# Kernel optimization log

Measured on AMD Instinct MI355X. Metric: run time of the kernel, lower is better.

The kernel has to match this reference:

```python
import jax, jax.numpy as jnp
import numpy as np
import math

B, N0, DEG = 32, 1584, 4
E = B * N0 * DEG
FIN, HID, EDIM, ROUTE, HEADS = 32, 64, 8, 16, 4
NEG = 0.2  # leaky_relu negative slope (alpha)
K1 = math.ceil(0.8 * N0)   # 1268 nodes/graph after pool1
K2 = math.ceil(0.8 * K1)   # 1015 after pool2
K3 = math.ceil(0.8 * K2)   # 812 after pool3


def _gatv2(x, src, dst, emask, edge_attr, Wl, bl, Wr, br, We, att, bo, num_nodes):
    # PyG GATv2Conv, concat=False (mean over heads), edge_dim, eval mode (no dropout)
    xl = (x @ Wl + bl).reshape(-1, HEADS, HID)            # source transform  [N,H,C]
    xr = (x @ Wr + br).reshape(-1, HEADS, HID)            # target transform  [N,H,C]
    ee = (edge_attr @ We).reshape(-1, HEADS, HID)         # edge transform    [E,H,C]
    m = jax.nn.leaky_relu(xl[src] + xr[dst] + ee, NEG)    # [E,H,C]
    logits = jnp.einsum('ehc,hc->eh', m, att)             # [E,H]
    logits = jnp.where(emask[:, None], logits, -jnp.inf)
    mx = jax.ops.segment_max(logits, dst, num_segments=num_nodes)
    mx = jnp.where(jnp.isfinite(mx), mx, 0.0)             # nodes w/o in-edges
    ex = jnp.where(emask[:, None], jnp.exp(logits - mx[dst]), 0.0)
    den = jax.ops.segment_sum(ex, dst, num_segments=num_nodes)
    alpha = ex / jnp.maximum(den[dst], 1e-16)             # segment softmax over dst
    out = jax.ops.segment_sum(alpha[:, :, None] * xl[src], dst, num_segments=num_nodes)
    return out.mean(axis=1) + bo                          # concat=False -> head mean


def _topk(x, src, dst, emask, w, n_per, k):
    # PyG TopKPooling(ratio=0.8): score = tanh(x.w/||w||); keep top-k per graph,
    # scale kept features by score; keep edges whose endpoints both survive.
    s = jnp.tanh((x @ w) / jnp.linalg.norm(w))            # [B*n_per]
    _, idx = jax.lax.top_k(s.reshape(B, n_per), k)        # [B,k]
    perm = (idx + jnp.arange(B)[:, None] * n_per).reshape(-1)
    x_new = x[perm] * s[perm][:, None]
    new_id = jnp.full((B * n_per,), -1, jnp.int32).at[perm].set(
        jnp.arange(B * k, dtype=jnp.int32))
    nsrc, ndst = new_id[src], new_id[dst]
    m = emask & (nsrc >= 0) & (ndst >= 0)
    return x_new, jnp.where(m, nsrc, 0), jnp.where(m, ndst, 0), m


def _readout(x, k):
    # global mean pool || global max pool (nodes are grouped per graph, k each)
    xb = x.reshape(B, k, HID)
    return jnp.concatenate([xb.mean(1), xb.max(1)], axis=1)


def _forward(x, edge_attr, edge_index,
             g1_Wl, g1_bl, g1_Wr, g1_br, g1_We, g1_att, g1_b,
             g2_Wl, g2_bl, g2_Wr, g2_br, g2_We, g2_att, g2_b,
             g3_Wl, g3_bl, g3_Wr, g3_br, g3_We, g3_att, g3_b,
             p1_w, p2_w, p3_w,
             fc1_W, fc1_b, fc2_W, fc2_b, fc3_W, fc3_b):
    src, dst = edge_index[0], edge_index[1]
    emask = jnp.ones((E,), bool)
    h = jax.nn.relu(_gatv2(x, src, dst, emask, edge_attr,
                           g1_Wl, g1_bl, g1_Wr, g1_br, g1_We, g1_att, g1_b, B * N0))
    h, src, dst, emask = _topk(h, src, dst, emask, p1_w, N0, K1)
    x1 = _readout(h, K1)
    h = jax.nn.relu(_gatv2(h, src, dst, emask, edge_attr,
                           g2_Wl, g2_bl, g2_Wr, g2_br, g2_We, g2_att, g2_b, B * K1))
    h, src, dst, emask = _topk(h, src, dst, emask, p2_w, K1, K2)
    x2 = _readout(h, K2)
    h = jax.nn.relu(_gatv2(h, src, dst, emask, edge_attr,
                           g3_Wl, g3_bl, g3_Wr, g3_br, g3_We, g3_att, g3_b, B * K2))
    h, src, dst, emask = _topk(h, src, dst, emask, p3_w, K2, K3)
    x3 = _readout(h, K3)
    r = x1 + x2 + x3                                      # [B, 2*HID]
    h = jax.nn.relu(r @ fc1_W + fc1_b)
    h = jax.nn.relu(h @ fc2_W + fc2_b)                    # dropout results unused in source
    return jax.nn.softmax(h @ fc3_W + fc3_b, axis=1)      # [B, ROUTE]


def setup_inputs() -> dict:
    key = jax.random.key(0)
    ks = iter(jax.random.split(key, 64))
    def nrm(shape, scale):
        return jax.random.normal(next(ks), shape, jnp.float32) * scale
    x = nrm((B * N0, FIN), 1.0)
    srcl = jax.random.randint(next(ks), (B, N0 * DEG), 0, N0)
    dstl = jax.random.randint(next(ks), (B, N0 * DEG), 0, N0)
    off = (jnp.arange(B) * N0)[:, None]
    edge_index = jnp.stack([(srcl + off).reshape(-1),
                            (dstl + off).reshape(-1)]).astype(jnp.int32)
    edge_attr = nrm((E, EDIM), 1.0)
    batch = jnp.repeat(jnp.arange(B, dtype=jnp.int32), N0)
    inp = {"x": x, "edge_attr": edge_attr, "edge_index": edge_index, "batch": batch}
    for li, fin in ((1, FIN), (2, HID), (3, HID)):
        g = 1.0 / np.sqrt(fin)
        inp[f"g{li}_Wl"] = nrm((fin, HEADS * HID), g)
        inp[f"g{li}_bl"] = nrm((HEADS * HID,), 0.02)
        inp[f"g{li}_Wr"] = nrm((fin, HEADS * HID), g)
        inp[f"g{li}_br"] = nrm((HEADS * HID,), 0.02)
        inp[f"g{li}_We"] = nrm((EDIM, HEADS * HID), 1.0 / np.sqrt(EDIM))
        inp[f"g{li}_att"] = nrm((HEADS, HID), 1.0 / np.sqrt(HID))
        inp[f"g{li}_b"] = nrm((HID,), 0.02)
    for li in (1, 2, 3):
        inp[f"p{li}_w"] = nrm((HID,), 1.0 / np.sqrt(HID))
    for fin, fout, nm in ((2 * HID, HID, "fc1"), (HID, HID, "fc2"), (HID, ROUTE, "fc3")):
        inp[f"{nm}_W"] = nrm((fin, fout), 1.0 / np.sqrt(fin))
        inp[f"{nm}_b"] = nrm((fout,), 0.02)
    return inp


def reference(x, edge_attr, edge_index, batch,
              g1_Wl, g1_bl, g1_Wr, g1_br, g1_We, g1_att, g1_b,
              g2_Wl, g2_bl, g2_Wr, g2_br, g2_We, g2_att, g2_b,
              g3_Wl, g3_bl, g3_Wr, g3_br, g3_We, g3_att, g3_b,
              p1_w, p2_w, p3_w,
              fc1_W, fc1_b, fc2_W, fc2_b, fc3_W, fc3_b):
    # batch is implicit: nodes are laid out grouped per graph with static sizes
    del batch
    return _forward(x, edge_attr, edge_index,
                    g1_Wl, g1_bl, g1_Wr, g1_br, g1_We, g1_att, g1_b,
                    g2_Wl, g2_bl, g2_Wr, g2_br, g2_We, g2_att, g2_b,
                    g3_Wl, g3_bl, g3_Wr, g3_br, g3_We, g3_att, g3_b,
                    p1_w, p2_w, p3_w,
                    fc1_W, fc1_b, fc2_W, fc2_b, fc3_W, fc3_b)
```

## Files before the change

kernel.cpp:

```cpp
#include <hip/hip_runtime.h>

typedef unsigned short u16;
typedef unsigned int u32;
typedef unsigned long long u64;

#define E_TOT 202752
#define NMAX  50688
#define HEADS 4
#define B_    32
#define MAXDEG 32

#define CDIV(a,b) (((a)+(b)-1)/(b))

__device__ __forceinline__ u32 ford(float f) {
  u32 u = __float_as_uint(f);
  return (u & 0x80000000u) ? ~u : (u | 0x80000000u);
}
__device__ __forceinline__ float ford_inv(u32 u) {
  u32 b = (u & 0x80000000u) ? (u ^ 0x80000000u) : ~u;
  return __uint_as_float(b);
}

template <int CTRL>
__device__ __forceinline__ float dpp_mov(float x) {
  return __int_as_float(__builtin_amdgcn_mov_dpp(__float_as_int(x), CTRL, 0xF, 0xF, false));
}
__device__ __forceinline__ float row16_sum(float v) {
  v += dpp_mov<0x121>(v);
  v += dpp_mov<0x122>(v);
  v += dpp_mov<0x124>(v);
  v += dpp_mov<0x128>(v);
  return v;
}

__global__ void k_edge_init_csr(const int* __restrict__ ei, int* __restrict__ src,
                                int* __restrict__ dst, int* __restrict__ em,
                                int* __restrict__ cnt, int* __restrict__ csr) {
  int e = blockIdx.x * blockDim.x + threadIdx.x;
  if (e >= E_TOT) return;
  int s = ei[e], d = ei[E_TOT + e];
  src[e] = s;
  dst[e] = d;
  em[e] = 1;
  int pos = atomicAdd(&cnt[d], 1);
  if (pos < MAXDEG) csr[d * MAXDEG + pos] = e;
}

template <int FIN>
__global__ void k_transform_t(const float* __restrict__ hin,
                              const float* __restrict__ Wl, const float* __restrict__ bl,
                              const float* __restrict__ Wr, const float* __restrict__ br,
                              float* __restrict__ xl, float* __restrict__ xr) {
  __shared__ float xs[FIN][20];
  int n0 = blockIdx.x * 16, j = threadIdx.x;
  for (int t = j; t < 16 * FIN; t += 256) {
    int nd = t >> (FIN == 32 ? 5 : 6), f = t & (FIN - 1);
    xs[f][nd] = hin[(size_t)(n0 + nd) * FIN + f];
  }
  __syncthreads();
  float al[16], ar[16];
  float blv = bl[j], brv = br[j];
#pragma unroll
  for (int t = 0; t < 16; ++t) { al[t] = blv; ar[t] = brv; }
  for (int i = 0; i < FIN; ++i) {
    float wl = Wl[i * 256 + j], wr = Wr[i * 256 + j];
    float4 x0 = *(const float4*)&xs[i][0];
    float4 x1 = *(const float4*)&xs[i][4];
    float4 x2 = *(const float4*)&xs[i][8];
    float4 x3 = *(const float4*)&xs[i][12];
    al[0]  += x0.x * wl; ar[0]  += x0.x * wr;
    al[1]  += x0.y * wl; ar[1]  += x0.y * wr;
    al[2]  += x0.z * wl; ar[2]  += x0.z * wr;
    al[3]  += x0.w * wl; ar[3]  += x0.w * wr;
    al[4]  += x1.x * wl; ar[4]  += x1.x * wr;
    al[5]  += x1.y * wl; ar[5]  += x1.y * wr;
    al[6]  += x1.z * wl; ar[6]  += x1.z * wr;
    al[7]  += x1.w * wl; ar[7]  += x1.w * wr;
    al[8]  += x2.x * wl; ar[8]  += x2.x * wr;
    al[9]  += x2.y * wl; ar[9]  += x2.y * wr;
    al[10] += x2.z * wl; ar[10] += x2.z * wr;
    al[11] += x2.w * wl; ar[11] += x2.w * wr;
    al[12] += x3.x * wl; ar[12] += x3.x * wr;
    al[13] += x3.y * wl; ar[13] += x3.y * wr;
    al[14] += x3.z * wl; ar[14] += x3.z * wr;
    al[15] += x3.w * wl; ar[15] += x3.w * wr;
  }
#pragma unroll
  for (int t = 0; t < 16; ++t) {
    xl[(size_t)(n0 + t) * 256 + j] = al[t];
    xr[(size_t)(n0 + t) * 256 + j] = ar[t];
  }
}

__global__ void k_gat_fused(const int* __restrict__ srcv, const int* __restrict__ cnt,
                            const int* __restrict__ csr, const float* __restrict__ ea,
                            const float* __restrict__ We, const float* __restrict__ att,
                            const float* __restrict__ xl, const float* __restrict__ xr,
                            const float* __restrict__ bias, const float* __restrict__ pwv,
                            float* __restrict__ out, float* __restrict__ sc,
                            int N, int npw) {
  int wid = blockIdx.x * 4 + (threadIdx.x >> 6);
  int lane = threadIdx.x & 63;
  int cg = lane & 15;
  int cb = (lane >> 4) * 64 + cg * 4;
  int n0 = wid * npw, n1 = min(N, n0 + npw);
  if (n0 >= N) return;
  float4 at4 = *(const float4*)(att + cb);
  float4 w0 = *(const float4*)(We + 0 * 256 + cb);
  float4 w1 = *(const float4*)(We + 1 * 256 + cb);
  float4 w2 = *(const float4*)(We + 2 * 256 + cb);
  float4 w3 = *(const float4*)(We + 3 * 256 + cb);
  float4 w4_ = *(const float4*)(We + 4 * 256 + cb);
  float4 w5 = *(const float4*)(We + 5 * 256 + cb);
  float4 w6 = *(const float4*)(We + 6 * 256 + cb);
  float4 w7 = *(const float4*)(We + 7 * 256 + cb);
  float4 bi4 = *(const float4*)(bias + cg * 4);
  float4 pw4 = *(const float4*)(pwv + cg * 4);
  float wn = pw4.x * pw4.x + pw4.y * pw4.y + pw4.z * pw4.z + pw4.w * pw4.w;
  wn += __shfl_xor(wn, 1, 64); wn += __shfl_xor(wn, 2, 64);
  wn += __shfl_xor(wn, 4, 64); wn += __shfl_xor(wn, 8, 64);
  float isq = 1.f / sqrtf(wn);

  for (int n = n0; n < n1; ++n) {
    int deg = min(cnt[n], MAXDEG);
    int e_l = 0, s_l = 0;
    if (lane < deg) { e_l = csr[n * MAXDEG + lane]; s_l = srcv[e_l]; }
    float4 xd4 = *(const float4*)(xr + (size_t)n * 256 + cb);
    float m = -INFINITY, l = 0.f;
    float ox = 0.f, oy = 0.f, oz = 0.f, ow = 0.f;
    for (int i0 = 0; i0 < deg; i0 += 4) {
      int c0 = deg - i0; if (c0 > 4) c0 = 4;
      float4 xs[4], a0[4], a1[4];
#pragma unroll
      for (int j = 0; j < 4; ++j) {
        int idx = (j < c0) ? (i0 + j) : i0;
        int e = __shfl(e_l, idx, 64);
        int s = __shfl(s_l, idx, 64);
        xs[j] = *(const float4*)(xl + (size_t)s * 256 + cb);
        a0[j] = *(const float4*)(ea + (size_t)e * 8);
        a1[j] = *(const float4*)(ea + (size_t)e * 8 + 4);
      }
#pragma unroll
      for (int j = 0; j < 4; ++j) {
        if (j < c0) {
          float e0 = a0[j].x * w0.x + a0[j].y * w1.x + a0[j].z * w2.x + a0[j].w * w3.x
                   + a1[j].x * w4_.x + a1[j].y * w5.x + a1[j].z * w6.x + a1[j].w * w7.x;
          float e1 = a0[j].x * w0.y + a0[j].y * w1.y + a0[j].z * w2.y + a0[j].w * w3.y
                   + a1[j].x * w4_.y + a1[j].y * w5.y + a1[j].z * w6.y + a1[j].w * w7.y;
          float e2 = a0[j].x * w0.z + a0[j].y * w1.z + a0[j].z * w2.z + a0[j].w * w3.z
                   + a1[j].x * w4_.z + a1[j].y * w5.z + a1[j].z * w6.z + a1[j].w * w7.z;
          float e3 = a0[j].x * w0.w + a0[j].y * w1.w + a0[j].z * w2.w + a0[j].w * w3.w
                   + a1[j].x * w4_.w + a1[j].y * w5.w + a1[j].z * w6.w + a1[j].w * w7.w;
          float m0 = xs[j].x + xd4.x + e0; m0 = (m0 >= 0.f) ? m0 : 0.2f * m0;
          float m1 = xs[j].y + xd4.y + e1; m1 = (m1 >= 0.f) ? m1 : 0.2f * m1;
          float m2 = xs[j].z + xd4.z + e2; m2 = (m2 >= 0.f) ? m2 : 0.2f * m2;
          float m3 = xs[j].w + xd4.w + e3; m3 = (m3 >= 0.f) ? m3 : 0.2f * m3;
          float v = at4.x * m0 + at4.y * m1 + at4.z * m2 + at4.w * m3;
          v = row16_sum(v);
          float nm = fmaxf(m, v);
          float scale = __expf(m - nm);
          float p = __expf(v - nm);
          ox = ox * scale + p * xs[j].x;
          oy = oy * scale + p * xs[j].y;
          oz = oz * scale + p * xs[j].z;
          ow = ow * scale + p * xs[j].w;
          l = l * scale + p;
          m = nm;
        }
      }
    }
    float inv = 0.25f / fmaxf(l, 1e-16f);
    float r0 = ox * inv, r1 = oy * inv, r2 = oz * inv, r3 = ow * inv;
    r0 += __shfl_xor(r0, 16, 64); r0 += __shfl_xor(r0, 32, 64);
    r1 += __shfl_xor(r1, 16, 64); r1 += __shfl_xor(r1, 32, 64);
    r2 += __shfl_xor(r2, 16, 64); r2 += __shfl_xor(r2, 32, 64);
    r3 += __shfl_xor(r3, 16, 64); r3 += __shfl_xor(r3, 32, 64);
    float rr0 = fmaxf(r0 + bi4.x, 0.f), rr1 = fmaxf(r1 + bi4.y, 0.f);
    float rr2 = fmaxf(r2 + bi4.z, 0.f), rr3 = fmaxf(r3 + bi4.w, 0.f);
    if (lane < 16) *(float4*)(out + (size_t)n * 64 + cg * 4) = float4{rr0, rr1, rr2, rr3};
    float dot = rr0 * pw4.x + rr1 * pw4.y + rr2 * pw4.z + rr3 * pw4.w;
    dot += __shfl_xor(dot, 1, 64);
    dot += __shfl_xor(dot, 2, 64);
    dot += __shfl_xor(dot, 4, 64);
    dot += __shfl_xor(dot, 8, 64);
    if (lane == 0) sc[n] = tanhf(dot * isq);
  }
}

__global__ __launch_bounds__(1024) void k_topk(const float* __restrict__ s, int n_per,
                                               int k, int npad,
                                               int* __restrict__ perm, int* __restrict__ new_id) {
  __shared__ u64 kv[2048];
  int b = blockIdx.x, tid = threadIdx.x;
  int base = b * n_per;
  for (int i = tid; i < n_per; i += 1024) new_id[base + i] = -1;
  for (int i = tid; i < npad; i += 1024) {
    u32 sk = (i < n_per) ? ford(s[base + i]) : 0u;
    kv[i] = ((u64)sk << 32) | (u32)(0xFFFFFFFFu - (u32)i);
  }
  __syncthreads();
  for (int kk = 2; kk <= npad; kk <<= 1) {
    for (int j = kk >> 1; j > 0; j >>= 1) {
      for (int i = tid; i < npad; i += 1024) {
        int ixj = i ^ j;
        if (ixj > i) {
          u64 a = kv[i], c = kv[ixj];
          bool after = a < c;
          bool doswap = ((i & kk) == 0) ? after : !after;
          if (doswap) { kv[i] = c; kv[ixj] = a; }
        }
      }
      __syncthreads();
    }
  }
  for (int r = tid; r < k; r += 1024) {
    int old = (int)(0xFFFFFFFFu - (u32)(kv[r] & 0xFFFFFFFFu));
    perm[b * k + r] = base + old;
    new_id[base + old] = b * k + r;
  }
}

__global__ void k_gather_ro(const float* __restrict__ hin, const float* __restrict__ s,
                            const int* __restrict__ perm, float* __restrict__ hout,
                            int k, float* __restrict__ rsum, u32* __restrict__ rmaxI) {
  __shared__ float ps[256], pm[256];
  int b = blockIdx.x, t = threadIdx.x;
  int i = blockIdx.y * 4 + (t >> 6);
  int c = t & 63;
  bool valid = i < k;
  float v = 0.f;
  if (valid) {
    int g = perm[b * k + i];
    v = hin[(size_t)g * 64 + c] * s[g];
    hout[((size_t)b * k + i) * 64 + c] = v;
  }
  ps[t] = valid ? v : 0.f;
  pm[t] = valid ? v : -INFINITY;
  __syncthreads();
  if (t < 64) {
    float s4 = ps[t] + ps[t + 64] + ps[t + 128] + ps[t + 192];
    float m4 = fmaxf(fmaxf(pm[t], pm[t + 64]), fmaxf(pm[t + 128], pm[t + 192]));
    atomicAdd(&rsum[b * 64 + t], s4);
    atomicMax(&rmaxI[b * 64 + t], ford(m4));
  }
}

__global__ void k_remap_csr(int* __restrict__ src, int* __restrict__ dst,
                            int* __restrict__ em, const int* __restrict__ new_id,
                            int* __restrict__ cnt, int* __restrict__ csr) {
  int e = blockIdx.x * blockDim.x + threadIdx.x;
  if (e >= E_TOT) return;
  int ns = new_id[src[e]], nd = new_id[dst[e]];
  int m = em[e] && ns >= 0 && nd >= 0;
  src[e] = m ? ns : 0;
  dst[e] = m ? nd : 0;
  em[e] = m;
  if (m) {
    int pos = atomicAdd(&cnt[nd], 1);
    if (pos < MAXDEG) csr[nd * MAXDEG + pos] = e;
  }
}

__global__ void k_mlp(const char* __restrict__ rblk,
                      const float* __restrict__ W1, const float* __restrict__ b1,
                      const float* __restrict__ W2, const float* __restrict__ b2,
                      const float* __restrict__ W3, const float* __restrict__ b3,
                      float* __restrict__ out) {
  __shared__ float v0[128], v1[64], v2[64], lgts[16];
  int b = blockIdx.x, t = threadIdx.x;
  const float* rs0 = (const float*)rblk;
  const u32*   rm0 = (const u32*)(rblk + 32 * 64 * 4);
  const float* rs1 = (const float*)(rblk + 32 * 128 * 4);
  const u32*   rm1 = (const u32*)(rblk + 32 * 128 * 4 + 32 * 64 * 4);
  const float* rs2 = (const float*)(rblk + 2 * 32 * 128 * 4);
  const u32*   rm2 = (const u32*)(rblk + 2 * 32 * 128 * 4 + 32 * 64 * 4);
  v0[t] = rs0[b * 64 + t] / 1268.f + rs1[b * 64 + t] / 1015.f + rs2[b * 64 + t] / 812.f;
  v0[64 + t] = ford_inv(rm0[b * 64 + t]) + ford_inv(rm1[b * 64 + t]) + ford_inv(rm2[b * 64 + t]);
  __syncthreads();
  float a = b1[t];
  for (int i = 0; i < 128; ++i) a += v0[i] * W1[i * 64 + t];
  v1[t] = fmaxf(a, 0.f);
  __syncthreads();
  a = b2[t];
  for (int i = 0; i < 64; ++i) a += v1[i] * W2[i * 64 + t];
  v2[t] = fmaxf(a, 0.f);
  __syncthreads();
  if (t < 16) {
    a = b3[t];
    for (int i = 0; i < 64; ++i) a += v2[i] * W3[i * 16 + t];
    lgts[t] = a;
  }
  __syncthreads();
  if (t == 0) {
    float m = lgts[0];
    for (int j = 1; j < 16; ++j) m = fmaxf(m, lgts[j]);
    float ex[16], sum = 0.f;
    for (int j = 0; j < 16; ++j) { ex[j] = expf(lgts[j] - m); sum += ex[j]; }
    for (int j = 0; j < 16; ++j) out[b * 16 + j] = ex[j] / sum;
  }
}

extern "C" void kernel_launch(void* const* d_in, const int* in_sizes, int n_in,
                              void* d_out, int out_size, void* d_ws, size_t ws_size,
                              hipStream_t stream) {
  (void)in_sizes; (void)n_in; (void)out_size; (void)ws_size;
  const float* x  = (const float*)d_in[0];
  const float* ea = (const float*)d_in[1];
  const int*   ei = (const int*)d_in[2];

  const float *gWl[3], *gbl[3], *gWr[3], *gbr[3], *gWe[3], *gatt[3], *gb[3], *pw[3];
  for (int l = 0; l < 3; ++l) {
    int p0 = 4 + 7 * l;
    gWl[l]  = (const float*)d_in[p0 + 0];
    gbl[l]  = (const float*)d_in[p0 + 1];
    gWr[l]  = (const float*)d_in[p0 + 2];
    gbr[l]  = (const float*)d_in[p0 + 3];
    gWe[l]  = (const float*)d_in[p0 + 4];
    gatt[l] = (const float*)d_in[p0 + 5];
    gb[l]   = (const float*)d_in[p0 + 6];
    pw[l]   = (const float*)d_in[25 + l];
  }
  const float* fc1W = (const float*)d_in[28];
  const float* fc1b = (const float*)d_in[29];
  const float* fc2W = (const float*)d_in[30];
  const float* fc2b = (const float*)d_in[31];
  const float* fc3W = (const float*)d_in[32];
  const float* fc3b = (const float*)d_in[33];

  char* w = (char*)d_ws;
  size_t off = 0;
  auto alloc = [&](size_t bytes) -> void* {
    void* p = w + off;
    off += (bytes + 255) & ~(size_t)255;
    return p;
  };
  float* hbuf = (float*)alloc((size_t)B_ * 1268 * 64 * 4);
  float* xl   = (float*)alloc((size_t)NMAX * 256 * 4);
  float* xr   = (float*)alloc((size_t)NMAX * 256 * 4);
  float* nacc = (float*)alloc((size_t)NMAX * 64 * 4);
  int*   cnt  = (int*)alloc((size_t)NMAX * 4);
  char*  rblk = (char*)alloc(3 * 32 * 128 * 4);
  int*   csr  = (int*)alloc((size_t)NMAX * MAXDEG * 4);
  float* sbuf = (float*)alloc((size_t)NMAX * 4);
  int* src    = (int*)alloc((size_t)E_TOT * 4);
  int* dst    = (int*)alloc((size_t)E_TOT * 4);
  int* em     = (int*)alloc((size_t)E_TOT * 4);
  int* new_id = (int*)alloc((size_t)NMAX * 4);
  int* perm   = (int*)alloc((size_t)32 * 1268 * 4);

  hipMemsetAsync(cnt, 0, (size_t)NMAX * 4, stream);
  hipMemsetAsync(rblk, 0, 3 * 32 * 128 * 4, stream);
  k_edge_init_csr<<<CDIV(E_TOT, 256), 256, 0, stream>>>(ei, src, dst, em, cnt, csr);

  const int Ns[3]    = {50688, 40576, 32480};
  const int npers[3] = {1584, 1268, 1015};
  const int ks[3]    = {1268, 1015, 812};
  const int npads[3] = {2048, 2048, 1024};
  const int GAT_BLOCKS = 2048;

  for (int l = 0; l < 3; ++l) {
    int N = Ns[l];
    const float* hin = (l == 0) ? x : hbuf;
    float* rsum = (float*)(rblk + l * 32 * 128 * 4);
    u32* rmaxI  = (u32*)(rblk + l * 32 * 128 * 4 + 32 * 64 * 4);
    if (l == 0)
      k_transform_t<32><<<N / 16, 256, 0, stream>>>(hin, gWl[l], gbl[l], gWr[l], gbr[l], xl, xr);
    else
      k_transform_t<64><<<N / 16, 256, 0, stream>>>(hin, gWl[l], gbl[l], gWr[l], gbr[l], xl, xr);
    int npw = CDIV(N, GAT_BLOCKS * 4);
    k_gat_fused<<<GAT_BLOCKS, 256, 0, stream>>>(src, cnt, csr, ea, gWe[l], gatt[l],
                                                xl, xr, gb[l], pw[l], nacc, sbuf, N, npw);
    k_topk<<<32, 1024, 0, stream>>>(sbuf, npers[l], ks[l], npads[l], perm, new_id);
    k_gather_ro<<<dim3(32, CDIV(ks[l], 4)), 256, 0, stream>>>(nacc, sbuf, perm, hbuf,
                                                              ks[l], rsum, rmaxI);
    if (l < 2) {
      hipMemsetAsync(cnt, 0, (size_t)NMAX * 4, stream);
      k_remap_csr<<<CDIV(E_TOT, 256), 256, 0, stream>>>(src, dst, em, new_id, cnt, csr);
    }
  }
  k_mlp<<<32, 64, 0, stream>>>(rblk, fc1W, fc1b, fc2W, fc2b, fc3W, fc3b, (float*)d_out);
}
```

Baseline: 522.7 us.

## Replace per-graph bitonic sort top-k with parallel rank counting

Swaps the single-block-per-graph bitonic sort over padded 2048 keys for a rank-by-counting kernel: each thread loads the graph's scores into shared memory and counts how many scores beat its own, with ties broken by index, which gives its output position directly. The grid becomes 32 graphs by several row blocks, so more CUs take part and the roughly sixty barrier-separated sort passes disappear. The cost is O(n^2) comparisons per graph, about 2.5M for the first layer, though these are cheap broadcast LDS reads. NaN scores would be ranked differently than under the ordered-key sort.

Result: slower. 565.4 us (+8.2%).

```diff
diff --git a/kernel.cpp b/kernel.cpp
--- a/kernel.cpp
+++ b/kernel.cpp
@@ -187,36 +187,26 @@
   }
 }
 
-__global__ __launch_bounds__(1024) void k_topk(const float* __restrict__ s, int n_per,
-                                               int k, int npad,
-                                               int* __restrict__ perm, int* __restrict__ new_id) {
-  __shared__ u64 kv[2048];
-  int b = blockIdx.x, tid = threadIdx.x;
-  int base = b * n_per;
-  for (int i = tid; i < n_per; i += 1024) new_id[base + i] = -1;
-  for (int i = tid; i < npad; i += 1024) {
-    u32 sk = (i < n_per) ? ford(s[base + i]) : 0u;
-    kv[i] = ((u64)sk << 32) | (u32)(0xFFFFFFFFu - (u32)i);
-  }
-  __syncthreads();
-  for (int kk = 2; kk <= npad; kk <<= 1) {
-    for (int j = kk >> 1; j > 0; j >>= 1) {
-      for (int i = tid; i < npad; i += 1024) {
-        int ixj = i ^ j;
-        if (ixj > i) {
-          u64 a = kv[i], c = kv[ixj];
-          bool after = a < c;
-          bool doswap = ((i & kk) == 0) ? after : !after;
-          if (doswap) { kv[i] = c; kv[ixj] = a; }
-        }
-      }
-      __syncthreads();
-    }
-  }
-  for (int r = tid; r < k; r += 1024) {
-    int old = (int)(0xFFFFFFFFu - (u32)(kv[r] & 0xFFFFFFFFu));
-    perm[b * k + r] = base + old;
-    new_id[base + old] = b * k + r;
+__global__ void k_rank(const float* __restrict__ s, int nper, int k,
+                       int* __restrict__ perm, int* __restrict__ new_id) {
+  __shared__ float sv[1584];
+  int g = blockIdx.x, t = threadIdx.x;
+  int base = g * nper;
+  for (int j = t; j < nper; j += 256) sv[j] = s[base + j];
+  __syncthreads();
+  int i = blockIdx.y * 256 + t;
+  if (i >= nper) return;
+  float si = sv[i];
+  int c = 0;
+  for (int j = 0; j < nper; ++j) {
+    float sj = sv[j];
+    c += (sj > si) || (sj == si && j < i);
+  }
+  if (c < k) {
+    perm[g * k + c] = base + i;
+    new_id[base + i] = g * k + c;
+  } else {
+    new_id[base + i] = -1;
   }
 }
 
@@ -355,7 +345,6 @@
   const int Ns[3]    = {50688, 40576, 32480};
   const int npers[3] = {1584, 1268, 1015};
   const int ks[3]    = {1268, 1015, 812};
-  const int npads[3] = {2048, 2048, 1024};
   const int GAT_BLOCKS = 2048;
 
   for (int l = 0; l < 3; ++l) {
@@ -370,7 +359,8 @@
     int npw = CDIV(N, GAT_BLOCKS * 4);
     k_gat_fused<<<GAT_BLOCKS, 256, 0, stream>>>(src, cnt, csr, ea, gWe[l], gatt[l],
                                                 xl, xr, gb[l], pw[l], nacc, sbuf, N, npw);
-    k_topk<<<32, 1024, 0, stream>>>(sbuf, npers[l], ks[l], npads[l], perm, new_id);
+    k_rank<<<dim3(32, CDIV(npers[l], 256)), 256, 0, stream>>>(sbuf, npers[l], ks[l],
+                                                              perm, new_id);
     k_gather_ro<<<dim3(32, CDIV(ks[l], 4)), 256, 0, stream>>>(nacc, sbuf, perm, hbuf,
                                                               ks[l], rsum, rmaxI);
     if (l < 2) {
```
